# Performance work log

Hardware: AMD Instinct MI355X
Metric: run time of the kernel (lower is better)

The kernel has to match this reference:

```python
import jax, jax.numpy as jnp
import numpy as np

B, HIST, PRED = 16, 336, 48
S = HIST + PRED                      # 384 = max_seq_length
H, NL, NH, FF = 768, 12, 12, 3072    # default BertConfig
SA_NH = 16                           # attention_heads arg for the extra SelfAttention
V = 40000                            # num_location_ids
NE = 8                               # num_experts
D_DAY, D_TIME, D_DOW, D_WD, D_LOC = 64, 64, 64, 32, 256
D_IN = D_DAY + D_TIME + D_DOW + D_WD + D_LOC + 1  # 481


def _ln(x, g, b, eps):
    m = jnp.mean(x, -1, keepdims=True)
    v = jnp.mean(jnp.square(x - m), -1, keepdims=True)
    return (x - m) * jax.lax.rsqrt(v + eps) * g + b


def _mha(x, qW, qb, kW, kb, vW, vb, nh):
    b_, s_, h_ = x.shape
    hd = h_ // nh
    q = (x @ qW + qb).reshape(b_, s_, nh, hd)
    k = (x @ kW + kb).reshape(b_, s_, nh, hd)
    v = (x @ vW + vb).reshape(b_, s_, nh, hd)
    scores = jnp.einsum('bqhd,bkhd->bhqk', q, k) / jnp.sqrt(jnp.float32(hd))
    probs = jax.nn.softmax(scores, axis=-1)
    return jnp.einsum('bhqk,bkhd->bqhd', probs, v).reshape(b_, s_, h_)


FLOAT_NAMES = ['day_emb', 'time_emb', 'dow_emb', 'wd_emb', 'loc_emb',
               'ln_in_g', 'ln_in_b', 'inp_W', 'inp_b', 'res_W', 'res_b',
               'sa_qW', 'sa_qb', 'sa_kW', 'sa_kb', 'sa_vW', 'sa_vb', 'sa_oW', 'sa_ob', 'sa_lng', 'sa_lnb',
               'pos_emb', 'tt_emb', 'be_lng', 'be_lnb',
               'bqW', 'bqb', 'bkW', 'bkb', 'bvW', 'bvb', 'boW', 'bob', 'balng', 'balnb',
               'bf1W', 'bf1b', 'bf2W', 'bf2b', 'bflng', 'bflnb',
               'moe_W', 'moe_b', 'gate_W', 'gate_b', 'out_W', 'out_b']


def _forward(floats, ints):
    (day_emb, time_emb, dow_emb, wd_emb, loc_emb,
     ln_in_g, ln_in_b, inp_W, inp_b, res_W, res_b,
     sa_qW, sa_qb, sa_kW, sa_kb, sa_vW, sa_vb, sa_oW, sa_ob, sa_lng, sa_lnb,
     pos_emb, tt_emb, be_lng, be_lnb,
     bqW, bqb, bkW, bkb, bvW, bvb, boW, bob, balng, balnb,
     bf1W, bf1b, bf2W, bf2b, bflng, bflnb,
     moe_W, moe_b, gate_W, gate_b, out_W, out_b) = floats
    isf, hloc, psf = ints

    def feat(f):
        return (day_emb[f[:, :, 0]], time_emb[f[:, :, 1]], dow_emb[f[:, :, 3]],
                wd_emb[f[:, :, 4]], f[:, :, 5].astype(jnp.float32)[..., None])
    hd_, ht_, hw_, hwd_, hdl = feat(isf)
    hist = jnp.concatenate([hd_, ht_, hw_, hwd_, hdl, loc_emb[hloc]], -1)
    fd_, ft_, fw_, fwd_, fdl = feat(psf)
    fut_loc = jnp.zeros((psf.shape[0], psf.shape[1], D_LOC), jnp.float32)  # unknown future locations
    fut = jnp.concatenate([fd_, ft_, fw_, fwd_, fdl, fut_loc], -1)
    x = jnp.concatenate([hist, fut], 1)            # [B,S,481]
    x = _ln(x, ln_in_g, ln_in_b, 1e-5)             # layer_norm on raw features (dropout = identity in eval)
    proj = x @ inp_W + inp_b                       # input_projection -> [B,S,768]
    res = x @ res_W + res_b                        # residual_fc -> [B,S,768]

    # extra SelfAttention block (16 heads) with post-LN residual
    ctx = _mha(proj, sa_qW, sa_qb, sa_kW, sa_kb, sa_vW, sa_vb, SA_NH)
    h = _ln(ctx @ sa_oW + sa_ob + proj, sa_lng, sa_lnb, 1e-5)

    # BERT encoder (inputs_embeds path): add position + token_type(0) embeddings, then 12 post-LN layers
    h = _ln(h + pos_emb[None] + tt_emb, be_lng, be_lnb, 1e-12)
    for i in range(NL):
        ctx = _mha(h, bqW[i], bqb[i], bkW[i], bkb[i], bvW[i], bvb[i], NH)
        a = _ln(ctx @ boW[i] + bob[i] + h, balng[i], balnb[i], 1e-12)
        ff = jax.nn.gelu(a @ bf1W[i] + bf1b[i], approximate=False) @ bf2W[i] + bf2b[i]
        h = _ln(ff + a, bflng[i], bflnb[i], 1e-12)

    # dense soft-MoE: every expert runs on every token, softmax-gated sum
    xf = h.reshape(-1, H)                                                 # [B*S, H]
    eo = jax.nn.gelu(jnp.einsum('nd,edh->neh', xf, moe_W) + moe_b[None], approximate=False)
    gp = jax.nn.softmax(xf @ gate_W + gate_b, axis=-1)                     # [B*S, E]
    moe_out = jnp.einsum('ne,neh->nh', gp, eo).reshape(h.shape)

    logits = (moe_out + res) @ out_W + out_b                               # [B,S,V]
    return logits[:, HIST:, :]                                             # predictions for future slots


def setup_inputs() -> dict:
    key = jax.random.key(0)
    ctr = [0]
    def nk():
        ctr[0] += 1
        return jax.random.fold_in(key, ctr[0])
    def nrm(shape, s=0.02):
        return jax.random.normal(nk(), shape, jnp.float32) * s
    p = {}
    p['input_seq_feature'] = jax.random.randint(nk(), (B, HIST, 6), 0, 2)
    p['historical_locations'] = jax.random.randint(nk(), (B, HIST), 0, V)
    p['predict_seq_feature'] = jax.random.randint(nk(), (B, PRED, 6), 0, 2)
    p['day_emb'] = nrm((75, D_DAY)); p['time_emb'] = nrm((48, D_TIME))
    p['dow_emb'] = nrm((7, D_DOW)); p['wd_emb'] = nrm((2, D_WD)); p['loc_emb'] = nrm((V, D_LOC))
    p['ln_in_g'] = jnp.ones((D_IN,), jnp.float32); p['ln_in_b'] = jnp.zeros((D_IN,), jnp.float32)
    p['inp_W'] = nrm((D_IN, H)); p['inp_b'] = jnp.zeros((H,), jnp.float32)
    p['res_W'] = nrm((D_IN, H)); p['res_b'] = jnp.zeros((H,), jnp.float32)
    for n in ['sa_qW', 'sa_kW', 'sa_vW', 'sa_oW']:
        p[n] = nrm((H, H))
    for n in ['sa_qb', 'sa_kb', 'sa_vb', 'sa_ob']:
        p[n] = jnp.zeros((H,), jnp.float32)
    p['sa_lng'] = jnp.ones((H,), jnp.float32); p['sa_lnb'] = jnp.zeros((H,), jnp.float32)
    p['pos_emb'] = nrm((S, H)); p['tt_emb'] = nrm((H,))
    p['be_lng'] = jnp.ones((H,), jnp.float32); p['be_lnb'] = jnp.zeros((H,), jnp.float32)
    for n in ['bqW', 'bkW', 'bvW', 'boW']:
        p[n] = nrm((NL, H, H))
    for n in ['bqb', 'bkb', 'bvb', 'bob']:
        p[n] = jnp.zeros((NL, H), jnp.float32)
    p['balng'] = jnp.ones((NL, H), jnp.float32); p['balnb'] = jnp.zeros((NL, H), jnp.float32)
    p['bf1W'] = nrm((NL, H, FF)); p['bf1b'] = jnp.zeros((NL, FF), jnp.float32)
    p['bf2W'] = nrm((NL, FF, H)); p['bf2b'] = jnp.zeros((NL, H), jnp.float32)
    p['bflng'] = jnp.ones((NL, H), jnp.float32); p['bflnb'] = jnp.zeros((NL, H), jnp.float32)
    p['moe_W'] = nrm((NE, H, H)); p['moe_b'] = jnp.zeros((NE, H), jnp.float32)
    p['gate_W'] = nrm((H, NE)); p['gate_b'] = jnp.zeros((NE,), jnp.float32)
    p['out_W'] = nrm((H, V)); p['out_b'] = jnp.zeros((V,), jnp.float32)
    return p


def reference(input_seq_feature, historical_locations, predict_seq_feature,
              day_emb, time_emb, dow_emb, wd_emb, loc_emb,
              ln_in_g, ln_in_b, inp_W, inp_b, res_W, res_b,
              sa_qW, sa_qb, sa_kW, sa_kb, sa_vW, sa_vb, sa_oW, sa_ob, sa_lng, sa_lnb,
              pos_emb, tt_emb, be_lng, be_lnb,
              bqW, bqb, bkW, bkb, bvW, bvb, boW, bob, balng, balnb,
              bf1W, bf1b, bf2W, bf2b, bflng, bflnb,
              moe_W, moe_b, gate_W, gate_b, out_W, out_b):
    floats = (day_emb, time_emb, dow_emb, wd_emb, loc_emb,
              ln_in_g, ln_in_b, inp_W, inp_b, res_W, res_b,
              sa_qW, sa_qb, sa_kW, sa_kb, sa_vW, sa_vb, sa_oW, sa_ob, sa_lng, sa_lnb,
              pos_emb, tt_emb, be_lng, be_lnb,
              bqW, bqb, bkW, bkb, bvW, bvb, boW, bob, balng, balnb,
              bf1W, bf1b, bf2W, bf2b, bflng, bflnb,
              moe_W, moe_b, gate_W, gate_b, out_W, out_b)
    ints = (input_seq_feature, historical_locations, predict_seq_feature)
    return _forward(floats, ints)
```

## Files before the change

kernel.cpp:

```cpp
#include <hip/hip_runtime.h>
#include <cstddef>
#include <math.h>

#define BB 16
#define HIST 336
#define PRED 48
#define SS 384
#define HH 768
#define NL 12
#define FF_ 3072
#define DIN 481
#define DINP 512
#define NE_ 8
#define VV 40000
#define VVP 40064

typedef __attribute__((ext_vector_type(8))) short short8;
typedef __attribute__((ext_vector_type(4))) float f32x4;
struct short4v { short x, y, z, w; };

__device__ __forceinline__ short f2bf(float f) {
    union { float f; unsigned u; } v; v.f = f;
    unsigned r = v.u + 0x7fff + ((v.u >> 16) & 1);
    return (short)(r >> 16);
}

using gvoid_t = const __attribute__((address_space(1))) void;
using svoid_t = __attribute__((address_space(3))) void;

template<int OP>
__global__ __launch_bounds__(256)
void gemm_bf16(const short* __restrict__ A, const short* __restrict__ Bt,
               const float* __restrict__ bias, const float* __restrict__ bias2,
               const float* __restrict__ bias3,
               void* __restrict__ Cout, void* __restrict__ Cout2,
               int Kp, int M, int ldc)
{
    __shared__ short As[2][128 * 64];
    __shared__ short Bs[2][128 * 64];
    const int tid  = threadIdx.x;
    const int lane = tid & 63;
    const int w    = tid >> 6;
    const int wr = w >> 1, wc = w & 1;
    const int lrow = lane & 15, lgrp = lane >> 4;
    const size_t rowBase = (size_t)blockIdx.y * 128;
    const size_t colBase = (size_t)blockIdx.x * 128;

    f32x4 acc[4][4];
    #pragma unroll
    for (int i = 0; i < 4; ++i)
        #pragma unroll
        for (int j = 0; j < 4; ++j)
            acc[i][j] = f32x4{0.f, 0.f, 0.f, 0.f};

    const int nkt = Kp >> 6;

    auto stage = [&](int buf, int kt) {
        const short* Ab = A  + rowBase * Kp + (size_t)kt * 64;
        const short* Bb = Bt + colBase * Kp + (size_t)kt * 64;
        #pragma unroll
        for (int c = 0; c < 4; ++c) {
            const int sidx = (w * 4 + c) * 64 + lane;
            const int r = sidx >> 3, sl = sidx & 7;
            const int sseg = sl ^ (r & 7);
            __builtin_amdgcn_global_load_lds(
                (gvoid_t*)(Ab + (size_t)r * Kp + sseg * 8),
                (svoid_t*)&As[buf][(w * 4 + c) * 512], 16, 0, 0);
            __builtin_amdgcn_global_load_lds(
                (gvoid_t*)(Bb + (size_t)r * Kp + sseg * 8),
                (svoid_t*)&Bs[buf][(w * 4 + c) * 512], 16, 0, 0);
        }
    };

    int cur = 0;
    stage(0, 0);
    __syncthreads();
    for (int kt = 0; kt < nkt; ++kt) {
        if (kt + 1 < nkt) stage(cur ^ 1, kt + 1);
        const short* as = As[cur];
        const short* bs = Bs[cur];
        #pragma unroll
        for (int kk = 0; kk < 2; ++kk) {
            short8 aF[4], bF[4];
            #pragma unroll
            for (int mi = 0; mi < 4; ++mi) {
                const int r = wr * 64 + mi * 16 + lrow;
                const int seg = (kk * 4 + lgrp) ^ (r & 7);
                aF[mi] = *(const short8*)&as[r * 64 + seg * 8];
            }
            #pragma unroll
            for (int ni = 0; ni < 4; ++ni) {
                const int r = wc * 64 + ni * 16 + lrow;
                const int seg = (kk * 4 + lgrp) ^ (r & 7);
                bF[ni] = *(const short8*)&bs[r * 64 + seg * 8];
            }
            #pragma unroll
            for (int mi = 0; mi < 4; ++mi)
                #pragma unroll
                for (int ni = 0; ni < 4; ++ni)
                    acc[mi][ni] = __builtin_amdgcn_mfma_f32_16x16x32_bf16(
                        aF[mi], bF[ni], acc[mi][ni], 0, 0, 0);
        }
        __syncthreads();
        cur ^= 1;
    }

    #pragma unroll
    for (int mi = 0; mi < 4; ++mi) {
        #pragma unroll
        for (int ni = 0; ni < 4; ++ni) {
            const int col = (int)colBase + wc * 64 + ni * 16 + lrow;
            if (col >= M) continue;
            const float* bp = bias; int bc = col;
            if (bias2 && col >= HH) {
                if (col < 2 * HH) { bp = bias2; bc = col - HH; }
                else              { bp = bias3; bc = col - 2 * HH; }
            }
            const float bz = bp[bc];
            #pragma unroll
            for (int j = 0; j < 4; ++j) {
                const size_t row = rowBase + wr * 64 + mi * 16 + lgrp * 4 + j;
                float v = acc[mi][ni][j] + bz;
                if (OP == 1 || OP == 4)
                    v = 0.5f * v * (1.f + erff(v * 0.70710678118654752f));
                if (OP == 4 || OP == 5) ((short*)Cout)[row * ldc + col] = f2bf(v);
                else                    ((float*)Cout)[row * ldc + col] = v;
                if (OP == 6)            ((short*)Cout2)[row * ldc + col] = f2bf(v);
            }
        }
    }
}

template<int HD>
__global__ __launch_bounds__(256)
void attn_mfma(const short* __restrict__ Qg, const short* __restrict__ Kg,
               const short* __restrict__ Vg, short* __restrict__ Og,
               int nh, int ldq, int ldo, float scale)
{
    constexpr int NI = HD / 16;
    constexpr int SEGS = HD / 8;
    __shared__ short Qs[64 * 64];
    __shared__ short Ks[64 * 64];
    __shared__ short Vt[64 * 72];
    __shared__ short Ps[4][16 * 80];
    int idx = blockIdx.x;
    const int qt = idx % 6; idx /= 6;
    const int h = idx % nh; idx /= nh;
    const int b = idx;
    const int tid = threadIdx.x;
    const int lane = tid & 63;
    const int w = tid >> 6;
    const int lrow = lane & 15, lgrp = lane >> 4;

    const short* Qbase = Qg + ((size_t)(b * SS + qt * 64)) * ldq + h * HD;
    #pragma unroll
    for (int t = 0; t < 2; ++t) {
        const int i = tid + t * 256;
        const int r = i >> 3, sg = i & 7;
        short8 v = {0, 0, 0, 0, 0, 0, 0, 0};
        if (sg < SEGS) v = *(const short8*)(Qbase + (size_t)r * ldq + sg * 8);
        *(short8*)&Qs[r * 64 + (sg ^ (r & 7)) * 8] = v;
    }

    float m_[4], l_[4];
    f32x4 o_[NI];
    #pragma unroll
    for (int j = 0; j < 4; ++j) { m_[j] = -1e30f; l_[j] = 0.f; }
    #pragma unroll
    for (int ni = 0; ni < NI; ++ni) o_[ni] = f32x4{0.f, 0.f, 0.f, 0.f};

    for (int kt = 0; kt < 6; ++kt) {
        const short* Kb2 = Kg + ((size_t)(b * SS + kt * 64)) * ldq + h * HD;
        const short* Vb2 = Vg + ((size_t)(b * SS + kt * 64)) * ldq + h * HD;
        __syncthreads();
        #pragma unroll
        for (int c = 0; c < 2; ++c) {
            const int r = (w * 2 + c) * 8 + (lane >> 3);
            const int sg = (lane & 7) ^ (r & 7);
            __builtin_amdgcn_global_load_lds(
                (gvoid_t*)(Kb2 + (size_t)r * ldq + sg * 8),
                (svoid_t*)&Ks[(w * 2 + c) * 512], 16, 0, 0);
        }
        for (int i = tid; i < 64 * SEGS; i += 256) {
            const int k = i & 63, sg = i >> 6;
            short8 v = *(const short8*)(Vb2 + (size_t)k * ldq + sg * 8);
            #pragma unroll
            for (int j2 = 0; j2 < 8; ++j2)
                Vt[(sg * 8 + j2) * 72 + k] = v[j2];
        }
        __syncthreads();

        f32x4 s[4];
        #pragma unroll
        for (int ni = 0; ni < 4; ++ni) s[ni] = f32x4{0.f, 0.f, 0.f, 0.f};
        #pragma unroll
        for (int kk = 0; kk < 2; ++kk) {
            const int ra = w * 16 + lrow;
            const short8 aF = *(const short8*)&Qs[ra * 64 + ((kk * 4 + lgrp) ^ (ra & 7)) * 8];
            #pragma unroll
            for (int ni = 0; ni < 4; ++ni) {
                const int rb = ni * 16 + lrow;
                const short8 bF = *(const short8*)&Ks[rb * 64 + ((kk * 4 + lgrp) ^ (rb & 7)) * 8];
                s[ni] = __builtin_amdgcn_mfma_f32_16x16x32_bf16(aF, bF, s[ni], 0, 0, 0);
            }
        }
        #pragma unroll
        for (int ni = 0; ni < 4; ++ni)
            #pragma unroll
            for (int j = 0; j < 4; ++j) s[ni][j] *= scale;

        #pragma unroll
        for (int j = 0; j < 4; ++j) {
            float tm = fmaxf(fmaxf(s[0][j], s[1][j]), fmaxf(s[2][j], s[3][j]));
            #pragma unroll
            for (int d = 1; d < 16; d <<= 1) tm = fmaxf(tm, __shfl_xor(tm, d));
            const float mn = fmaxf(m_[j], tm);
            const float r2 = __expf(m_[j] - mn);
            float p[4], ps = 0.f;
            #pragma unroll
            for (int ni = 0; ni < 4; ++ni) { p[ni] = __expf(s[ni][j] - mn); ps += p[ni]; }
            #pragma unroll
            for (int d = 1; d < 16; d <<= 1) ps += __shfl_xor(ps, d);
            l_[j] = l_[j] * r2 + ps;
            m_[j] = mn;
            #pragma unroll
            for (int ni = 0; ni < NI; ++ni) o_[ni][j] *= r2;
            #pragma unroll
            for (int ni = 0; ni < 4; ++ni)
                Ps[w][(lgrp * 4 + j) * 80 + ni * 16 + lrow] = f2bf(p[ni]);
        }

        #pragma unroll
        for (int kk = 0; kk < 2; ++kk) {
            const short8 aP = *(const short8*)&Ps[w][lrow * 80 + kk * 32 + lgrp * 8];
            #pragma unroll
            for (int ni = 0; ni < NI; ++ni) {
                const int d0 = ni * 16 + lrow;
                const short8 bV = *(const short8*)&Vt[d0 * 72 + (kk * 4 + lgrp) * 8];
                o_[ni] = __builtin_amdgcn_mfma_f32_16x16x32_bf16(aP, bV, o_[ni], 0, 0, 0);
            }
        }
    }

    const size_t orow0 = (size_t)(b * SS + qt * 64 + w * 16);
    #pragma unroll
    for (int j = 0; j < 4; ++j) {
        const float inv = 1.f / l_[j];
        #pragma unroll
        for (int ni = 0; ni < NI; ++ni)
            Og[(orow0 + lgrp * 4 + j) * ldo + h * HD + ni * 16 + lrow] =
                f2bf(o_[ni][j] * inv);
    }
}

__global__ __launch_bounds__(256)
void transpose_cvt_b(const float* __restrict__ W, short* __restrict__ Wt,
                     int K, int M, int Kp, size_t sStride, size_t dStride)
{
    __shared__ float tile[32][33];
    const float* src = W + blockIdx.z * sStride;
    short* dst = Wt + blockIdx.z * dStride;
    const int m0 = blockIdx.x * 32, k0 = blockIdx.y * 32;
    const int tx = threadIdx.x, ty = threadIdx.y;
    #pragma unroll
    for (int i = 0; i < 4; ++i) {
        int k = k0 + ty + i * 8, m = m0 + tx;
        tile[ty + i * 8][tx] = (k < K && m < M) ? src[(size_t)k * M + m] : 0.f;
    }
    __syncthreads();
    #pragma unroll
    for (int i = 0; i < 4; ++i) {
        int m = m0 + ty + i * 8, k = k0 + tx;
        dst[(size_t)m * Kp + k] = f2bf(tile[tx][ty + i * 8]);
    }
}

__global__ __launch_bounds__(256)
void prep_layer_w(const float* __restrict__ bq, const float* __restrict__ bk,
                  const float* __restrict__ bv, const float* __restrict__ bo,
                  const float* __restrict__ f1, const float* __restrict__ f2,
                  short* __restrict__ qkvT, short* __restrict__ oT,
                  short* __restrict__ f1T, short* __restrict__ f2T)
{
    __shared__ float tile[32][33];
    int id = blockIdx.x;
    const float* src; short* dst; int K, M, tm, tk;
    if (id < 1728) {
        const int mat = id / 576, r = id % 576;
        src = mat == 0 ? bq : (mat == 1 ? bk : bv);
        dst = qkvT + (size_t)mat * HH * HH;
        K = HH; M = HH; tm = r % 24; tk = r / 24;
    } else if (id < 2304) {
        const int r = id - 1728;
        src = bo; dst = oT; K = HH; M = HH; tm = r % 24; tk = r / 24;
    } else if (id < 4608) {
        const int r = id - 2304;
        src = f1; dst = f1T; K = HH; M = FF_; tm = r % 96; tk = r / 96;
    } else {
        const int r = id - 4608;
        src = f2; dst = f2T; K = FF_; M = HH; tm = r % 24; tk = r / 24;
    }
    const int m0 = tm * 32, k0 = tk * 32;
    const int tx = threadIdx.x & 31, ty = threadIdx.x >> 5;
    #pragma unroll
    for (int i = 0; i < 4; ++i) {
        int k = k0 + ty + i * 8, m = m0 + tx;
        tile[ty + i * 8][tx] = src[(size_t)k * M + m];
    }
    __syncthreads();
    #pragma unroll
    for (int i = 0; i < 4; ++i) {
        int m = m0 + ty + i * 8, k = k0 + tx;
        dst[(size_t)m * K + k] = f2bf(tile[tx][ty + i * 8]);
    }
}

__global__ __launch_bounds__(256)
void cvt_bf16(const float* __restrict__ src, short* __restrict__ dst, int n4)
{
    int i = blockIdx.x * 256 + threadIdx.x;
    if (i >= n4) return;
    float4 v = reinterpret_cast<const float4*>(src)[i];
    short4v o = { f2bf(v.x), f2bf(v.y), f2bf(v.z), f2bf(v.w) };
    reinterpret_cast<short4v*>(dst)[i] = o;
}

__global__ __launch_bounds__(512)
void build_x(const int* __restrict__ isf, const int* __restrict__ hloc,
             const int* __restrict__ psf,
             const float* __restrict__ dayE, const float* __restrict__ timeE,
             const float* __restrict__ dowE, const float* __restrict__ wdE,
             const float* __restrict__ locE,
             const float* __restrict__ g, const float* __restrict__ b2,
             short* __restrict__ xb)
{
    const int tok = blockIdx.x;
    const int b = tok / SS, s = tok % SS;
    const int tid = threadIdx.x;
    __shared__ float red[512];
    const int* f;
    int loc = -1;
    if (s < HIST) { f = isf + (b * HIST + s) * 6; loc = hloc[b * HIST + s]; }
    else          { f = psf + (b * PRED + (s - HIST)) * 6; }
    float val = 0.f;
    if (tid < DIN) {
        int c = tid;
        if      (c < 64)  val = dayE[f[0] * 64 + c];
        else if (c < 128) val = timeE[f[1] * 64 + (c - 64)];
        else if (c < 192) val = dowE[f[3] * 64 + (c - 128)];
        else if (c < 224) val = wdE[f[4] * 32 + (c - 192)];
        else if (c == 224) val = (float)f[5];
        else val = (loc >= 0) ? locE[(size_t)loc * 256 + (c - 225)] : 0.f;
    }
    red[tid] = (tid < DIN) ? val : 0.f;
    __syncthreads();
    for (int o = 256; o > 0; o >>= 1) { if (tid < o) red[tid] += red[tid + o]; __syncthreads(); }
    float mean = red[0] / (float)DIN;
    __syncthreads();
    float d = (tid < DIN) ? (val - mean) : 0.f;
    red[tid] = d * d;
    __syncthreads();
    for (int o = 256; o > 0; o >>= 1) { if (tid < o) red[tid] += red[tid + o]; __syncthreads(); }
    float rstd = rsqrtf(red[0] / (float)DIN + 1e-5f);
    if (tid < DINP)
        xb[(size_t)tok * DINP + tid] =
            (tid < DIN) ? f2bf((val - mean) * rstd * g[tid] + b2[tid]) : (short)0;
}

__global__ __launch_bounds__(256)
void ln768(float* __restrict__ out, short* __restrict__ outb,
           const float* __restrict__ in1, const float* __restrict__ in2,
           const float* __restrict__ pos, const float* __restrict__ tt,
           const float* __restrict__ g, const float* __restrict__ b2,
           float eps)
{
    const int D = HH;
    const int row = blockIdx.x;
    const int s = row % SS;
    __shared__ float buf[HH];
    __shared__ float red[256];
    const int tid = threadIdx.x;
    float partial = 0.f;
    #pragma unroll
    for (int i = 0; i < 3; ++i) {
        int c = tid + i * 256;
        float v = in1[(size_t)row * D + c];
        if (in2) v += in2[(size_t)row * D + c];
        if (pos) v += pos[(size_t)s * D + c];
        if (tt)  v += tt[c];
        buf[c] = v;
        partial += v;
    }
    red[tid] = partial; __syncthreads();
    for (int o = 128; o > 0; o >>= 1) { if (tid < o) red[tid] += red[tid + o]; __syncthreads(); }
    float mean = red[0] / (float)D;
    __syncthreads();
    float p2 = 0.f;
    #pragma unroll
    for (int i = 0; i < 3; ++i) { float d = buf[tid + i * 256] - mean; p2 += d * d; }
    red[tid] = p2; __syncthreads();
    for (int o = 128; o > 0; o >>= 1) { if (tid < o) red[tid] += red[tid + o]; __syncthreads(); }
    float rstd = rsqrtf(red[0] / (float)D + eps);
    #pragma unroll
    for (int i = 0; i < 3; ++i) {
        int c = tid + i * 256;
        float v = (buf[c] - mean) * rstd * g[c] + b2[c];
        out[(size_t)row * D + c] = v;
        if (outb) outb[(size_t)row * D + c] = f2bf(v);
    }
}

__global__ void gather_fut_f32(const float* __restrict__ src, float* __restrict__ dst, int D)
{
    const int r = blockIdx.x;
    const int b = r / PRED, t = r % PRED;
    const int srow = b * SS + HIST + t;
    for (int c = threadIdx.x; c < D; c += blockDim.x)
        dst[(size_t)r * D + c] = src[(size_t)srow * D + c];
}
__global__ void gather_fut_b16(const short* __restrict__ src, short* __restrict__ dst, int D)
{
    const int r = blockIdx.x;
    const int b = r / PRED, t = r % PRED;
    const int srow = b * SS + HIST + t;
    for (int c = threadIdx.x; c < D; c += blockDim.x)
        dst[(size_t)r * D + c] = src[(size_t)srow * D + c];
}

__global__ __launch_bounds__(256)
void gate_kernel(const float* __restrict__ Xf, const float* __restrict__ Wg,
                 const float* __restrict__ bg, float* __restrict__ out)
{
    const int row = blockIdx.x;
    const int tid = threadIdx.x;
    float a[NE_] = {};
    for (int k = tid; k < HH; k += 256) {
        float xv = Xf[(size_t)row * HH + k];
        #pragma unroll
        for (int e = 0; e < NE_; ++e) a[e] = fmaf(xv, Wg[k * NE_ + e], a[e]);
    }
    __shared__ float red[256];
    #pragma unroll
    for (int e = 0; e < NE_; ++e) {
        red[tid] = a[e]; __syncthreads();
        for (int o = 128; o > 0; o >>= 1) { if (tid < o) red[tid] += red[tid + o]; __syncthreads(); }
        if (tid == 0) out[(size_t)row * NE_ + e] = red[0] + bg[e];
        __syncthreads();
    }
}

__global__ void gate_softmax(float* __restrict__ gate)
{
    const int r = blockIdx.x * blockDim.x + threadIdx.x;
    if (r >= BB * PRED) return;
    float* p = gate + (size_t)r * NE_;
    float mx = p[0];
    for (int e = 1; e < NE_; ++e) mx = fmaxf(mx, p[e]);
    float s = 0.f, v[NE_];
    for (int e = 0; e < NE_; ++e) { v[e] = __expf(p[e] - mx); s += v[e]; }
    for (int e = 0; e < NE_; ++e) p[e] = v[e] / s;
}

__global__ __launch_bounds__(256)
void moe_reduce(const float* __restrict__ eo, const float* __restrict__ gp,
                float* __restrict__ futm)
{
    const int row = blockIdx.x;
    float g[NE_];
    #pragma unroll
    for (int e = 0; e < NE_; ++e) g[e] = gp[row * NE_ + e];
    for (int c = threadIdx.x; c < HH; c += 256) {
        float s = futm[(size_t)row * HH + c];
        #pragma unroll
        for (int e = 0; e < NE_; ++e)
            s = fmaf(g[e], eo[(size_t)row * (NE_ * HH) + e * HH + c], s);
        futm[(size_t)row * HH + c] = s;
    }
}

extern "C" void kernel_launch(void* const* d_in, const int* in_sizes, int n_in,
                              void* d_out, int out_size, void* d_ws, size_t ws_size,
                              hipStream_t stream)
{
    const int*   isf   = (const int*)  d_in[0];
    const int*   hloc  = (const int*)  d_in[1];
    const int*   psf   = (const int*)  d_in[2];
    const float* dayE  = (const float*)d_in[3];
    const float* timeE = (const float*)d_in[4];
    const float* dowE  = (const float*)d_in[5];
    const float* wdE   = (const float*)d_in[6];
    const float* locE  = (const float*)d_in[7];
    const float* ln_g  = (const float*)d_in[8];
    const float* ln_b  = (const float*)d_in[9];
    const float* inpW  = (const float*)d_in[10];
    const float* inpB  = (const float*)d_in[11];
    const float* resW  = (const float*)d_in[12];
    const float* resB  = (const float*)d_in[13];
    const float* saqW  = (const float*)d_in[14];
    const float* sakW  = (const float*)d_in[15];
    const float* savW  = (const float*)d_in[16];
    const float* saoW  = (const float*)d_in[17];
    const float* saqB  = (const float*)d_in[18];
    const float* sakB  = (const float*)d_in[19];
    const float* savB  = (const float*)d_in[20];
    const float* saoB  = (const float*)d_in[21];
    const float* salnG = (const float*)d_in[22];
    const float* salnB = (const float*)d_in[23];
    const float* posE  = (const float*)d_in[24];
    const float* ttE   = (const float*)d_in[25];
    const float* belnG = (const float*)d_in[26];
    const float* belnB = (const float*)d_in[27];
    const float* bqW   = (const float*)d_in[28];
    const float* bkW   = (const float*)d_in[29];
    const float* bvW   = (const float*)d_in[30];
    const float* boW   = (const float*)d_in[31];
    const float* bqB   = (const float*)d_in[32];
    const float* bkB   = (const float*)d_in[33];
    const float* bvB   = (const float*)d_in[34];
    const float* boB   = (const float*)d_in[35];
    const float* balnG = (const float*)d_in[36];
    const float* balnB = (const float*)d_in[37];
    const float* bf1W  = (const float*)d_in[38];
    const float* bf1B  = (const float*)d_in[39];
    const float* bf2W  = (const float*)d_in[40];
    const float* bf2B  = (const float*)d_in[41];
    const float* bflnG = (const float*)d_in[42];
    const float* bflnB = (const float*)d_in[43];
    const float* moeW  = (const float*)d_in[44];
    const float* moeB  = (const float*)d_in[45];
    const float* gateW = (const float*)d_in[46];
    const float* gateB = (const float*)d_in[47];
    const float* outW  = (const float*)d_in[48];
    const float* outB  = (const float*)d_in[49];

    const int N6 = BB * SS;
    const int NF = BB * PRED;

    char* base = (char*)d_ws;
    size_t off = 0;
    auto alloc = [&](size_t bytes) -> void* {
        void* p = base + off;
        off = (off + bytes + 255) & ~(size_t)255;
        return p;
    };

    short* xb     = (short*)alloc((size_t)N6 * DINP * 2);
    short* hb     = (short*)alloc((size_t)N6 * HH * 2);
    short* Ob     = (short*)alloc((size_t)N6 * HH * 2);
    short* QKVb   = (short*)alloc((size_t)N6 * 3 * HH * 2);
    float* Cb     = (float*)alloc((size_t)N6 * HH * 4);
    short* ffb    = (short*)alloc((size_t)N6 * FF_ * 2);
    float* Hh     = (float*)alloc((size_t)N6 * HH * 4);
    float* Abuf   = (float*)alloc((size_t)N6 * HH * 4);
    short* inpWt  = (short*)alloc((size_t)HH * DINP * 2);
    short* resWt  = (short*)alloc((size_t)HH * DINP * 2);
    short* saWt   = (short*)alloc((size_t)3 * HH * HH * 2);
    short* saoWt  = (short*)alloc((size_t)HH * HH * 2);
    short* lqkvWt = (short*)alloc((size_t)3 * HH * HH * 2);
    short* loWt   = (short*)alloc((size_t)HH * HH * 2);
    short* lf1Wt  = (short*)alloc((size_t)FF_ * HH * 2);
    short* lf2Wt  = (short*)alloc((size_t)HH * FF_ * 2);
    float* futh   = (float*)alloc((size_t)NF * HH * 4);
    float* futm   = (float*)alloc((size_t)NF * HH * 4);
    float* futg   = (float*)alloc((size_t)NF * NE_ * 4);

    short* outWt = QKVb;
    short* moeWt = outWt + (size_t)VVP * HH;
    short* futhb = moeWt + (size_t)NE_ * HH * HH;
    short* futxb = futhb + (size_t)NF * HH;
    short* futmb = futxb + (size_t)NF * DINP;

    build_x<<<N6, 512, 0, stream>>>(isf, hloc, psf, dayE, timeE, dowE, wdE, locE,
                                    ln_g, ln_b, xb);

    dim3 tb(32, 8);
    transpose_cvt_b<<<dim3(HH/32, DINP/32, 1), tb, 0, stream>>>(inpW, inpWt, DIN, HH, DINP, 0, 0);
    transpose_cvt_b<<<dim3(HH/32, DINP/32, 1), tb, 0, stream>>>(resW, resWt, DIN, HH, DINP, 0, 0);
    transpose_cvt_b<<<dim3(HH/32, HH/32, 1), tb, 0, stream>>>(saqW, saWt,                   HH, HH, HH, 0, 0);
    transpose_cvt_b<<<dim3(HH/32, HH/32, 1), tb, 0, stream>>>(sakW, saWt + (size_t)HH*HH,   HH, HH, HH, 0, 0);
    transpose_cvt_b<<<dim3(HH/32, HH/32, 1), tb, 0, stream>>>(savW, saWt + (size_t)2*HH*HH, HH, HH, HH, 0, 0);
    transpose_cvt_b<<<dim3(HH/32, HH/32, 1), tb, 0, stream>>>(saoW, saoWt, HH, HH, HH, 0, 0);

    gemm_bf16<6><<<dim3(HH/128, N6/128), 256, 0, stream>>>(
        xb, inpWt, inpB, nullptr, nullptr, Abuf, hb, DINP, HH, HH);

    gemm_bf16<5><<<dim3(3*HH/128, N6/128), 256, 0, stream>>>(
        hb, saWt, saqB, sakB, savB, QKVb, nullptr, HH, 3*HH, 3*HH);
    attn_mfma<48><<<BB*16*6, 256, 0, stream>>>(
        QKVb, QKVb + HH, QKVb + 2*HH, Ob, 16, 3*HH, HH, 1.f / sqrtf(48.f));
    gemm_bf16<0><<<dim3(HH/128, N6/128), 256, 0, stream>>>(
        Ob, saoWt, saoB, nullptr, nullptr, Cb, nullptr, HH, HH, HH);
    ln768<<<N6, 256, 0, stream>>>(Hh, nullptr, Cb, Abuf, nullptr, nullptr,
                                  salnG, salnB, 1e-5f);

    ln768<<<N6, 256, 0, stream>>>(Hh, hb, Hh, nullptr, posE, ttE,
                                  belnG, belnB, 1e-12f);

    for (int i = 0; i < NL; ++i) {
        const size_t wo = (size_t)i * HH * HH;
        const size_t bo = (size_t)i * HH;
        prep_layer_w<<<6912, 256, 0, stream>>>(
            bqW + wo, bkW + wo, bvW + wo, boW + wo,
            bf1W + (size_t)i * HH * FF_, bf2W + (size_t)i * FF_ * HH,
            lqkvWt, loWt, lf1Wt, lf2Wt);

        gemm_bf16<5><<<dim3(3*HH/128, N6/128), 256, 0, stream>>>(
            hb, lqkvWt, bqB + bo, bkB + bo, bvB + bo, QKVb, nullptr, HH, 3*HH, 3*HH);
        attn_mfma<64><<<BB*12*6, 256, 0, stream>>>(
            QKVb, QKVb + HH, QKVb + 2*HH, Ob, 12, 3*HH, HH, 0.125f);
        gemm_bf16<0><<<dim3(HH/128, N6/128), 256, 0, stream>>>(
            Ob, loWt, boB + bo, nullptr, nullptr, Cb, nullptr, HH, HH, HH);
        ln768<<<N6, 256, 0, stream>>>(Abuf, hb, Cb, Hh, nullptr, nullptr,
                                      balnG + bo, balnB + bo, 1e-12f);
        gemm_bf16<4><<<dim3(FF_/128, N6/128), 256, 0, stream>>>(
            hb, lf1Wt, bf1B + (size_t)i * FF_, nullptr, nullptr, ffb, nullptr, HH, FF_, FF_);
        gemm_bf16<0><<<dim3(HH/128, N6/128), 256, 0, stream>>>(
            ffb, lf2Wt, bf2B + bo, nullptr, nullptr, Cb, nullptr, FF_, HH, HH);
        ln768<<<N6, 256, 0, stream>>>(Hh, hb, Cb, Abuf, nullptr, nullptr,
                                      bflnG + bo, bflnB + bo, 1e-12f);
    }

    gather_fut_f32<<<NF, 256, 0, stream>>>(Hh, futh, HH);
    gather_fut_b16<<<NF, 256, 0, stream>>>(hb, futhb, HH);
    gather_fut_b16<<<NF, 256, 0, stream>>>(xb, futxb, DINP);

    gemm_bf16<0><<<dim3(HH/128, NF/128), 256, 0, stream>>>(
        futxb, resWt, resB, nullptr, nullptr, futm, nullptr, DINP, HH, HH);

    gate_kernel<<<NF, 256, 0, stream>>>(futh, gateW, gateB, futg);
    gate_softmax<<<3, 256, 0, stream>>>(futg);

    transpose_cvt_b<<<dim3(HH/32, HH/32, NE_), tb, 0, stream>>>(
        moeW, moeWt, HH, HH, HH, (size_t)HH*HH, (size_t)HH*HH);
    gemm_bf16<1><<<dim3(NE_*HH/128, NF/128), 256, 0, stream>>>(
        futhb, moeWt, moeB, nullptr, nullptr, Hh, nullptr, HH, NE_*HH, NE_*HH);
    moe_reduce<<<NF, 256, 0, stream>>>(Hh, futg, futm);

    {
        int n4 = (int)((size_t)NF * HH / 4);
        cvt_bf16<<<(n4 + 255) / 256, 256, 0, stream>>>(futm, futmb, n4);
    }
    transpose_cvt_b<<<dim3(VVP/32, HH/32, 1), tb, 0, stream>>>(
        outW, outWt, HH, VV, HH, 0, 0);
    gemm_bf16<0><<<dim3(VVP/128, NF/128), 256, 0, stream>>>(
        futmb, outWt, outB, nullptr, nullptr, (float*)d_out, nullptr, HH, VV, VV);
}
```

Before: 3.735 ms.

## Triple-buffer GEMM LDS pipeline with 8 waves and MFMA priority

The bf16 GEMM moves from 4 to 8 waves per 128x128 block, with each wave computing a 64x32 sub-tile. The LDS staging grows to three buffers, and a vmcnt-based wait with one barrier per k-step replaces the double buffer and its two syncs. s_setprio is raised around the MFMA burst. This aims to hide global-to-LDS latency and raise latency tolerance, at the cost of more LDS (96KB), which caps occupancy at one block per CU, and duplicated A-fragment reads across wave columns.

```diff
diff --git a/kernel.cpp b/kernel.cpp
--- a/kernel.cpp
+++ b/kernel.cpp
@@ -29,28 +29,28 @@
 using svoid_t = __attribute__((address_space(3))) void;
 
 template<int OP>
-__global__ __launch_bounds__(256)
+__global__ __launch_bounds__(512, 1)
 void gemm_bf16(const short* __restrict__ A, const short* __restrict__ Bt,
                const float* __restrict__ bias, const float* __restrict__ bias2,
                const float* __restrict__ bias3,
                void* __restrict__ Cout, void* __restrict__ Cout2,
                int Kp, int M, int ldc)
 {
-    __shared__ short As[2][128 * 64];
-    __shared__ short Bs[2][128 * 64];
+    __shared__ short As[3][128 * 64];
+    __shared__ short Bs[3][128 * 64];
     const int tid  = threadIdx.x;
     const int lane = tid & 63;
     const int w    = tid >> 6;
-    const int wr = w >> 1, wc = w & 1;
+    const int wr = w >> 2, wc = w & 3;
     const int lrow = lane & 15, lgrp = lane >> 4;
     const size_t rowBase = (size_t)blockIdx.y * 128;
     const size_t colBase = (size_t)blockIdx.x * 128;
 
-    f32x4 acc[4][4];
+    f32x4 acc[4][2];
     #pragma unroll
     for (int i = 0; i < 4; ++i)
         #pragma unroll
-        for (int j = 0; j < 4; ++j)
+        for (int j = 0; j < 2; ++j)
             acc[i][j] = f32x4{0.f, 0.f, 0.f, 0.f};
 
     const int nkt = Kp >> 6;
@@ -59,29 +59,41 @@
         const short* Ab = A  + rowBase * Kp + (size_t)kt * 64;
         const short* Bb = Bt + colBase * Kp + (size_t)kt * 64;
         #pragma unroll
-        for (int c = 0; c < 4; ++c) {
-            const int sidx = (w * 4 + c) * 64 + lane;
-            const int r = sidx >> 3, sl = sidx & 7;
+        for (int c = 0; c < 2; ++c) {
+            const int chunk = w * 2 + c;
+            const int sidx = chunk * 512 + lane * 8;
+            const int r = sidx >> 6, sl = (sidx & 63) >> 3;
             const int sseg = sl ^ (r & 7);
             __builtin_amdgcn_global_load_lds(
                 (gvoid_t*)(Ab + (size_t)r * Kp + sseg * 8),
-                (svoid_t*)&As[buf][(w * 4 + c) * 512], 16, 0, 0);
+                (svoid_t*)&As[buf][chunk * 512], 16, 0, 0);
+        }
+        #pragma unroll
+        for (int c = 0; c < 2; ++c) {
+            const int chunk = w * 2 + c;
+            const int sidx = chunk * 512 + lane * 8;
+            const int r = sidx >> 6, sl = (sidx & 63) >> 3;
+            const int sseg = sl ^ (r & 7);
             __builtin_amdgcn_global_load_lds(
                 (gvoid_t*)(Bb + (size_t)r * Kp + sseg * 8),
-                (svoid_t*)&Bs[buf][(w * 4 + c) * 512], 16, 0, 0);
+                (svoid_t*)&Bs[buf][chunk * 512], 16, 0, 0);
         }
     };
 
-    int cur = 0;
     stage(0, 0);
-    __syncthreads();
+    if (nkt > 1) stage(1, 1);
+
     for (int kt = 0; kt < nkt; ++kt) {
-        if (kt + 1 < nkt) stage(cur ^ 1, kt + 1);
-        const short* as = As[cur];
-        const short* bs = Bs[cur];
+        if (kt + 1 < nkt) { asm volatile("s_waitcnt vmcnt(4)" ::: "memory"); }
+        else              { asm volatile("s_waitcnt vmcnt(0)" ::: "memory"); }
+        __builtin_amdgcn_s_barrier();
+        if (kt + 2 < nkt) stage((kt + 2) % 3, kt + 2);
+
+        const short* as = As[kt % 3];
+        const short* bs = Bs[kt % 3];
         #pragma unroll
         for (int kk = 0; kk < 2; ++kk) {
-            short8 aF[4], bF[4];
+            short8 aF[4], bF[2];
             #pragma unroll
             for (int mi = 0; mi < 4; ++mi) {
                 const int r = wr * 64 + mi * 16 + lrow;
@@ -89,27 +101,27 @@
                 aF[mi] = *(const short8*)&as[r * 64 + seg * 8];
             }
             #pragma unroll
-            for (int ni = 0; ni < 4; ++ni) {
-                const int r = wc * 64 + ni * 16 + lrow;
+            for (int ni = 0; ni < 2; ++ni) {
+                const int r = wc * 32 + ni * 16 + lrow;
                 const int seg = (kk * 4 + lgrp) ^ (r & 7);
                 bF[ni] = *(const short8*)&bs[r * 64 + seg * 8];
             }
+            __builtin_amdgcn_s_setprio(1);
             #pragma unroll
             for (int mi = 0; mi < 4; ++mi)
                 #pragma unroll
-                for (int ni = 0; ni < 4; ++ni)
+                for (int ni = 0; ni < 2; ++ni)
                     acc[mi][ni] = __builtin_amdgcn_mfma_f32_16x16x32_bf16(
                         aF[mi], bF[ni], acc[mi][ni], 0, 0, 0);
-        }
-        __syncthreads();
-        cur ^= 1;
+            __builtin_amdgcn_s_setprio(0);
+        }
     }
 
     #pragma unroll
     for (int mi = 0; mi < 4; ++mi) {
         #pragma unroll
-        for (int ni = 0; ni < 4; ++ni) {
-            const int col = (int)colBase + wc * 64 + ni * 16 + lrow;
+        for (int ni = 0; ni < 2; ++ni) {
+            const int col = (int)colBase + wc * 32 + ni * 16 + lrow;
             if (col >= M) continue;
             const float* bp = bias; int bc = col;
             if (bias2 && col >= HH) {
@@ -581,14 +593,14 @@
     transpose_cvt_b<<<dim3(HH/32, HH/32, 1), tb, 0, stream>>>(savW, saWt + (size_t)2*HH*HH, HH, HH, HH, 0, 0);
     transpose_cvt_b<<<dim3(HH/32, HH/32, 1), tb, 0, stream>>>(saoW, saoWt, HH, HH, HH, 0, 0);
 
-    gemm_bf16<6><<<dim3(HH/128, N6/128), 256, 0, stream>>>(
+    gemm_bf16<6><<<dim3(HH/128, N6/128), 512, 0, stream>>>(
         xb, inpWt, inpB, nullptr, nullptr, Abuf, hb, DINP, HH, HH);
 
-    gemm_bf16<5><<<dim3(3*HH/128, N6/128), 256, 0, stream>>>(
+    gemm_bf16<5><<<dim3(3*HH/128, N6/128), 512, 0, stream>>>(
         hb, saWt, saqB, sakB, savB, QKVb, nullptr, HH, 3*HH, 3*HH);
     attn_mfma<48><<<BB*16*6, 256, 0, stream>>>(
         QKVb, QKVb + HH, QKVb + 2*HH, Ob, 16, 3*HH, HH, 1.f / sqrtf(48.f));
-    gemm_bf16<0><<<dim3(HH/128, N6/128), 256, 0, stream>>>(
+    gemm_bf16<0><<<dim3(HH/128, N6/128), 512, 0, stream>>>(
         Ob, saoWt, saoB, nullptr, nullptr, Cb, nullptr, HH, HH, HH);
     ln768<<<N6, 256, 0, stream>>>(Hh, nullptr, Cb, Abuf, nullptr, nullptr,
                                   salnG, salnB, 1e-5f);
@@ -604,17 +616,17 @@
             bf1W + (size_t)i * HH * FF_, bf2W + (size_t)i * FF_ * HH,
             lqkvWt, loWt, lf1Wt, lf2Wt);
 
-        gemm_bf16<5><<<dim3(3*HH/128, N6/128), 256, 0, stream>>>(
+        gemm_bf16<5><<<dim3(3*HH/128, N6/128), 512, 0, stream>>>(
             hb, lqkvWt, bqB + bo, bkB + bo, bvB + bo, QKVb, nullptr, HH, 3*HH, 3*HH);
         attn_mfma<64><<<BB*12*6, 256, 0, stream>>>(
             QKVb, QKVb + HH, QKVb + 2*HH, Ob, 12, 3*HH, HH, 0.125f);
-        gemm_bf16<0><<<dim3(HH/128, N6/128), 256, 0, stream>>>(
+        gemm_bf16<0><<<dim3(HH/128, N6/128), 512, 0, stream>>>(
             Ob, loWt, boB + bo, nullptr, nullptr, Cb, nullptr, HH, HH, HH);
         ln768<<<N6, 256, 0, stream>>>(Abuf, hb, Cb, Hh, nullptr, nullptr,
                                       balnG + bo, balnB + bo, 1e-12f);
-        gemm_bf16<4><<<dim3(FF_/128, N6/128), 256, 0, stream>>>(
+        gemm_bf16<4><<<dim3(FF_/128, N6/128), 512, 0, stream>>>(
             hb, lf1Wt, bf1B + (size_t)i * FF_, nullptr, nullptr, ffb, nullptr, HH, FF_, FF_);
-        gemm_bf16<0><<<dim3(HH/128, N6/128), 256, 0, stream>>>(
+        gemm_bf16<0><<<dim3(HH/128, N6/128), 512, 0, stream>>>(
             ffb, lf2Wt, bf2B + bo, nullptr, nullptr, Cb, nullptr, FF_, HH, HH);
         ln768<<<N6, 256, 0, stream>>>(Hh, hb, Cb, Abuf, nullptr, nullptr,
                                       bflnG + bo, bflnB + bo, 1e-12f);
@@ -624,7 +636,7 @@
     gather_fut_b16<<<NF, 256, 0, stream>>>(hb, futhb, HH);
     gather_fut_b16<<<NF, 256, 0, stream>>>(xb, futxb, DINP);
 
-    gemm_bf16<0><<<dim3(HH/128, NF/128), 256, 0, stream>>>(
+    gemm_bf16<0><<<dim3(HH/128, NF/128), 512, 0, stream>>>(
         futxb, resWt, resB, nullptr, nullptr, futm, nullptr, DINP, HH, HH);
 
     gate_kernel<<<NF, 256, 0, stream>>>(futh, gateW, gateB, futg);
@@ -632,7 +644,7 @@
 
     transpose_cvt_b<<<dim3(HH/32, HH/32, NE_), tb, 0, stream>>>(
         moeW, moeWt, HH, HH, HH, (size_t)HH*HH, (size_t)HH*HH);
-    gemm_bf16<1><<<dim3(NE_*HH/128, NF/128), 256, 0, stream>>>(
+    gemm_bf16<1><<<dim3(NE_*HH/128, NF/128), 512, 0, stream>>>(
         futhb, moeWt, moeB, nullptr, nullptr, Hh, nullptr, HH, NE_*HH, NE_*HH);
     moe_reduce<<<NF, 256, 0, stream>>>(Hh, futg, futm);
 
@@ -642,6 +654,6 @@
     }
     transpose_cvt_b<<<dim3(VVP/32, HH/32, 1), tb, 0, stream>>>(
         outW, outWt, HH, VV, HH, 0, 0);
-    gemm_bf16<0><<<dim3(VVP/128, NF/128), 256, 0, stream>>>(
+    gemm_bf16<0><<<dim3(VVP/128, NF/128), 512, 0, stream>>>(
         futmb, outWt, outB, nullptr, nullptr, (float*)d_out, nullptr, HH, VV, VV);
 }
```

Result: slower. 4.649 ms (+24.5%).
